# Kernel optimization log

Measured on AMD Instinct MI355X. Metric: run time of the kernel, lower is better.

Reference implementation:

```python
import jax, jax.numpy as jnp
import numpy as np

B, S, D = 2, 2048, 1024
H = 16
HD = D // H

def setup_inputs() -> dict:
    key = jax.random.key(0)
    k1, k2, k3 = jax.random.split(key, 3)
    x = jax.random.normal(k1, (B, S, D), dtype=jnp.float32)
    w_attn = jax.random.normal(k2, (D, 3 * D), dtype=jnp.float32) * (1.0 / np.sqrt(D))
    b_attn = jnp.zeros((3 * D,), dtype=jnp.float32)
    w_proj = jax.random.normal(k3, (D, D), dtype=jnp.float32) * (1.0 / np.sqrt(D))
    b_proj = jnp.zeros((D,), dtype=jnp.float32)
    return {"x": x, "w_attn": w_attn, "b_attn": b_attn, "w_proj": w_proj, "b_proj": b_proj}

def reference(x, w_attn, b_attn, w_proj, b_proj):
    bsz, seq_len, embed_dim = x.shape
    qkv = x @ w_attn + b_attn                      # [B,S,3D]
    q, k, v = jnp.split(qkv, 3, axis=-1)
    # [B,S,D] -> [B,H,S,HD]
    def heads(t):
        return t.reshape(bsz, seq_len, H, HD).transpose(0, 2, 1, 3)
    q, k, v = heads(q), heads(k), heads(v)
    scale = 1.0 / np.sqrt(HD)
    att = jnp.einsum('bhqd,bhkd->bhqk', q, k) * scale  # [B,H,S,S]
    causal = jnp.tril(jnp.ones((seq_len, seq_len), dtype=bool))
    att = jnp.where(causal[None, None], att, jnp.float32(-jnp.inf))
    att = jax.nn.softmax(att, axis=-1)
    y = jnp.einsum('bhqk,bhkd->bhqd', att, v)          # [B,H,S,HD]
    y = y.transpose(0, 2, 1, 3).reshape(bsz, seq_len, embed_dim)
    return y @ w_proj + b_proj
```

## Files before the change

kernel.cpp:

```cpp
#include <hip/hip_runtime.h>
#include <hip/hip_bf16.h>
#include <math.h>

typedef __bf16 bf16x8 __attribute__((ext_vector_type(8)));
typedef __bf16 bf16x4 __attribute__((ext_vector_type(4)));
typedef float f32x4 __attribute__((ext_vector_type(4)));

#define LOG2E 1.44269504088896340736f

#define SEQ 2048
#define DMODEL 1024
#define NH 16
#define HD 64

__device__ __forceinline__ void gl2lds16(const void* g, void* l) {
  __builtin_amdgcn_global_load_lds((__attribute__((address_space(1))) void*)g,
                                   (__attribute__((address_space(3))) void*)l,
                                   16, 0, 0);
}

__device__ __forceinline__ unsigned compute_flag_local(const unsigned* __restrict__ x,
                                                       int* cnt) {
  int c = 0;
  for (int i = threadIdx.x; i < 4096; i += 256) {
    unsigned e = (x[i] >> 23) & 0xFF;
    c += (e >= 0x70 && e <= 0x8F) ? 1 : 0;
  }
  cnt[threadIdx.x] = c;
  __syncthreads();
  for (int s = 128; s > 0; s >>= 1) {
    if ((int)threadIdx.x < s) cnt[threadIdx.x] += cnt[threadIdx.x + s];
    __syncthreads();
  }
  return (cnt[0] > 2048) ? 1u : 0u;
}

__device__ __forceinline__ void transpose_tile(const void* __restrict__ in,
                                               __hip_bfloat16* __restrict__ out,
                                               int R, int C, int c0, int r0, bool f32,
                                               __hip_bfloat16 (*tile)[65]) {
  const int tx = threadIdx.x & 63, ty = threadIdx.x >> 6;
#pragma unroll
  for (int i = 0; i < 16; ++i) {
    int r = ty + i * 4;
    long idx = (long)(r0 + r) * C + c0 + tx;
    tile[r][tx] = f32 ? __float2bfloat16(((const float*)in)[idx])
                      : ((const __hip_bfloat16*)in)[idx];
  }
  __syncthreads();
#pragma unroll
  for (int i = 0; i < 16; ++i) {
    int r = ty + i * 4;
    out[(long)(c0 + r) * R + r0 + tx] = tile[tx][r];
  }
}

__global__ void prep_all(const void* __restrict__ x, const void* __restrict__ w_attn,
                         const void* __restrict__ w_proj,
                         __hip_bfloat16* __restrict__ x_bf,
                         __hip_bfloat16* __restrict__ wT_attn,
                         __hip_bfloat16* __restrict__ wT_proj,
                         unsigned* __restrict__ flag) {
  __shared__ int cnt[256];
  __shared__ __hip_bfloat16 tile[64][65];
  const unsigned f = compute_flag_local((const unsigned*)x, cnt);
  const int bid = blockIdx.x;
  if (bid == 0 && threadIdx.x == 0) flag[0] = f;

  if (bid < 4096) {
    const int i = (bid * 256 + threadIdx.x) * 4;
    if (f) {
      const float4 v = *(const float4*)((const float*)x + i);
      x_bf[i + 0] = __float2bfloat16(v.x);
      x_bf[i + 1] = __float2bfloat16(v.y);
      x_bf[i + 2] = __float2bfloat16(v.z);
      x_bf[i + 3] = __float2bfloat16(v.w);
    } else {
      *(bf16x4*)(x_bf + i) = *(const bf16x4*)((const __hip_bfloat16*)x + i);
    }
  } else if (bid < 4096 + 768) {
    const int b2 = bid - 4096;
    const int c0 = (b2 % 48) * 64, r0 = (b2 / 48) * 64;
    transpose_tile(w_attn, wT_attn, 1024, 3072, c0, r0, f != 0, tile);
  } else {
    const int b3 = bid - 4096 - 768;
    const int c0 = (b3 % 16) * 64, r0 = (b3 / 16) * 64;
    transpose_tile(w_proj, wT_proj, 1024, 1024, c0, r0, f != 0, tile);
  }
}

template <int MODE>
__global__ __launch_bounds__(256, 3) void gemm_bt(
    const __hip_bfloat16* __restrict__ A, const __hip_bfloat16* __restrict__ Bt,
    const void* __restrict__ bias, void* __restrict__ C,
    __hip_bfloat16* __restrict__ q_ws, __hip_bfloat16* __restrict__ k_ws,
    __hip_bfloat16* __restrict__ vt_ws, int M, int N, int K,
    const unsigned* __restrict__ flag) {
  alignas(16) __shared__ __hip_bfloat16 lA[128 * 64];
  alignas(16) __shared__ __hip_bfloat16 lB[128 * 64];
  const int tid = threadIdx.x;
  const int wave = tid >> 6, lane = tid & 63;
  const int l15 = lane & 15, lq = lane >> 4;
  const int m0 = blockIdx.y * 128, n0 = blockIdx.x * 128;
  const int wrow = (wave >> 1) * 64, wcol = (wave & 1) * 64;

  const int rs = lane >> 3;
  const int cs = lane & 7;
  const int gch = cs ^ rs;
  const __hip_bfloat16* ap0 = A + (long)(m0 + wave * 32 + rs) * K + gch * 8;
  const __hip_bfloat16* bp0 = Bt + (long)(n0 + wave * 32 + rs) * K + gch * 8;

  f32x4 acc[4][4];
#pragma unroll
  for (int i = 0; i < 4; ++i)
#pragma unroll
    for (int j = 0; j < 4; ++j) acc[i][j] = {0.f, 0.f, 0.f, 0.f};

  for (int k0 = 0; k0 < K; k0 += 64) {
    __syncthreads();
#pragma unroll
    for (int i = 0; i < 4; ++i) {
      gl2lds16(ap0 + (long)(i * 8) * K + k0, lA + (wave * 4 + i) * 512);
      gl2lds16(bp0 + (long)(i * 8) * K + k0, lB + (wave * 4 + i) * 512);
    }
    __syncthreads();
#pragma unroll
    for (int ks = 0; ks < 2; ++ks) {
      bf16x8 af[4], bfr[4];
#pragma unroll
      for (int i = 0; i < 4; ++i) {
        const int p = wrow + 16 * i + l15;
        af[i] = *(const bf16x8*)(lA + p * 64 + (((ks * 4 + lq) ^ (l15 & 7)) * 8));
      }
#pragma unroll
      for (int j = 0; j < 4; ++j) {
        const int p = wcol + 16 * j + l15;
        bfr[j] = *(const bf16x8*)(lB + p * 64 + (((ks * 4 + lq) ^ (l15 & 7)) * 8));
      }
#pragma unroll
      for (int i = 0; i < 4; ++i)
#pragma unroll
        for (int j = 0; j < 4; ++j)
          acc[i][j] = __builtin_amdgcn_mfma_f32_16x16x32_bf16(af[i], bfr[j], acc[i][j], 0, 0, 0);
    }
  }

  const bool f32in = (*flag != 0);
  const bool outf32 = (MODE == 0) && f32in;
  const float KSCL = 0.125f * LOG2E;
#pragma unroll
  for (int i = 0; i < 4; ++i) {
    const int row = m0 + wrow + 16 * i + lq * 4;
#pragma unroll
    for (int j = 0; j < 4; ++j) {
      const int col = n0 + wcol + 16 * j + l15;
      const float bv = f32in ? ((const float*)bias)[col]
                             : __bfloat162float(((const __hip_bfloat16*)bias)[col]);
#pragma unroll
      for (int r = 0; r < 4; ++r) {
        const float v = acc[i][j][r] + bv;
        const int rr = row + r;
        if (MODE == 0) {
          if (outf32)
            ((float*)C)[(long)rr * N + col] = v;
          else
            ((__hip_bfloat16*)C)[(long)rr * N + col] = __float2bfloat16(v);
        } else {
          const int which = col >> 10;
          const int f = col & 1023;
          const int h = f >> 6, d = f & 63;
          const int b = rr >> 11, s = rr & 2047;
          const long bh = (long)b * NH + h;
          if (which == 0)
            q_ws[(bh * SEQ + s) * HD + d] = __float2bfloat16(v);
          else if (which == 1)
            k_ws[(bh * SEQ + s) * HD + d] = __float2bfloat16(v * KSCL);
          else {
            const int w = s & 31;
            const int wl = w & 15;
            const int sig = (w >> 4) ? (2 * (wl & ~3) + 4 + (wl & 3))
                                     : (2 * (wl & ~3) + (wl & 3));
            const int sp = (s & ~31) | sig;
            vt_ws[(bh * HD + d) * SEQ + sp] = __float2bfloat16(v);
          }
        }
      }
    }
  }
}

__global__ __launch_bounds__(256, 4) void attn_fused(
    const __hip_bfloat16* __restrict__ q_ws, const __hip_bfloat16* __restrict__ k_ws,
    const __hip_bfloat16* __restrict__ vt_ws, __hip_bfloat16* __restrict__ y_ws) {
  alignas(16) __shared__ __hip_bfloat16 lK[2][64 * 64];
  alignas(16) __shared__ __hip_bfloat16 lV[2][64 * 64];
  const int tid = threadIdx.x, wave = tid >> 6, lane = tid & 63;
  const int l15 = lane & 15, lq = lane >> 4;
  const int qt = 31 - (blockIdx.x >> 5);
  const int bh = blockIdx.x & 31;
  const int q0 = qt * 64;
  const int nkt = qt + 1;
  const __hip_bfloat16* Qb = q_ws + (long)bh * SEQ * HD;
  const __hip_bfloat16* Kb = k_ws + (long)bh * SEQ * HD;
  const __hip_bfloat16* Vb = vt_ws + (long)bh * HD * SEQ;
  const int b = bh >> 4, h = bh & 15;

  const int qrow = q0 + wave * 16 + l15;
  const bf16x8 qa0 = *(const bf16x8*)(Qb + (long)qrow * HD + lq * 8);
  const bf16x8 qa1 = *(const bf16x8*)(Qb + (long)qrow * HD + 32 + lq * 8);

  f32x4 accO[4];
  f32x4 accL;
#pragma unroll
  for (int j = 0; j < 4; ++j) accO[j] = {0.f, 0.f, 0.f, 0.f};
  accL = {0.f, 0.f, 0.f, 0.f};
  const __bf16 one = (__bf16)1.0f;
  const bf16x8 onesA = {one, one, one, one, one, one, one, one};

  const int p0 = wave * 16 + (lane >> 3);
  const int cl = lane & 7;

#pragma unroll
  for (int i = 0; i < 2; ++i) {
    const int p = p0 + i * 8;
    const int c = cl ^ (p & 7);
    gl2lds16(Kb + (long)p * HD + c * 8, &lK[0][(wave * 16 + i * 8) * 64]);
    gl2lds16(Vb + (long)p * SEQ + c * 8, &lV[0][(wave * 16 + i * 8) * 64]);
  }
  __syncthreads();

#pragma unroll 1
  for (int kt = 0; kt < nkt; ++kt) {
    const int buf = kt & 1;
    if (kt + 1 < nkt) {
      const int kb = (kt + 1) * 64;
#pragma unroll
      for (int i = 0; i < 2; ++i) {
        const int p = p0 + i * 8;
        const int c = cl ^ (p & 7);
        gl2lds16(Kb + (long)(kb + p) * HD + c * 8, &lK[buf ^ 1][(wave * 16 + i * 8) * 64]);
        gl2lds16(Vb + (long)p * SEQ + kb + c * 8, &lV[buf ^ 1][(wave * 16 + i * 8) * 64]);
      }
    }
    const __hip_bfloat16* lKb = lK[buf];
    const __hip_bfloat16* lVb = lV[buf];

    f32x4 st[4];
#pragma unroll
    for (int t = 0; t < 4; ++t) {
      st[t] = {0.f, 0.f, 0.f, 0.f};
      const int pp = t * 16 + l15;
      const bf16x8 kb0 = *(const bf16x8*)(lKb + (pp * 8 + (lq ^ (pp & 7))) * 8);
      const bf16x8 kb1 = *(const bf16x8*)(lKb + (pp * 8 + ((4 + lq) ^ (pp & 7))) * 8);
      st[t] = __builtin_amdgcn_mfma_f32_16x16x32_bf16(kb0, qa0, st[t], 0, 0, 0);
      st[t] = __builtin_amdgcn_mfma_f32_16x16x32_bf16(kb1, qa1, st[t], 0, 0, 0);
    }

    const bool diag = (kt == nkt - 1);
    const int qloc = wave * 16 + l15;
    bf16x8 pb[2];
#pragma unroll
    for (int c = 0; c < 2; ++c) {
#pragma unroll
      for (int t2 = 0; t2 < 2; ++t2) {
        const int tt = c * 2 + t2;
#pragma unroll
        for (int r = 0; r < 4; ++r) {
          float pv = exp2f(st[tt][r]);
          if (diag) {
            const int colloc = tt * 16 + lq * 4 + r;
            pv = (colloc <= qloc) ? pv : 0.f;
          }
          pb[c][t2 * 4 + r] = (__bf16)pv;
        }
      }
    }

#pragma unroll
    for (int j = 0; j < 4; ++j) {
      const int d = j * 16 + l15;
      const bf16x8 va0 = *(const bf16x8*)(lVb + (d * 8 + (lq ^ (d & 7))) * 8);
      const bf16x8 va1 = *(const bf16x8*)(lVb + (d * 8 + ((4 + lq) ^ (d & 7))) * 8);
      accO[j] = __builtin_amdgcn_mfma_f32_16x16x32_bf16(va0, pb[0], accO[j], 0, 0, 0);
      accO[j] = __builtin_amdgcn_mfma_f32_16x16x32_bf16(va1, pb[1], accO[j], 0, 0, 0);
    }
    accL = __builtin_amdgcn_mfma_f32_16x16x32_bf16(onesA, pb[0], accL, 0, 0, 0);
    accL = __builtin_amdgcn_mfma_f32_16x16x32_bf16(onesA, pb[1], accL, 0, 0, 0);
    __syncthreads();
  }

  const float inv = 1.f / accL[0];
  const int s = q0 + wave * 16 + l15;
  __hip_bfloat16* yb = y_ws + (long)(b * SEQ + s) * DMODEL + h * HD;
#pragma unroll
  for (int j = 0; j < 4; ++j) {
    bf16x4 o;
#pragma unroll
    for (int r = 0; r < 4; ++r) o[r] = (__bf16)(accO[j][r] * inv);
    *(bf16x4*)(yb + j * 16 + lq * 4) = o;
  }
}

extern "C" void kernel_launch(void* const* d_in, const int* in_sizes, int n_in,
                              void* d_out, int out_size, void* d_ws, size_t ws_size,
                              hipStream_t stream) {
  const void* x = d_in[0];
  const void* w_attn = d_in[1];
  const void* b_attn = d_in[2];
  const void* w_proj = d_in[3];
  const void* b_proj = d_in[4];

  char* ws = (char*)d_ws;
  const size_t MB = 1024 * 1024;
  unsigned* flag = (unsigned*)ws;
  __hip_bfloat16* wT_attn = (__hip_bfloat16*)(ws + 1 * MB);
  __hip_bfloat16* wT_proj = (__hip_bfloat16*)(ws + 7 * MB);
  __hip_bfloat16* x_bf = (__hip_bfloat16*)(ws + 9 * MB);
  __hip_bfloat16* q_ws = (__hip_bfloat16*)(ws + 17 * MB);
  __hip_bfloat16* k_ws = (__hip_bfloat16*)(ws + 25 * MB);
  __hip_bfloat16* vt_ws = (__hip_bfloat16*)(ws + 33 * MB);
  __hip_bfloat16* y_ws = (__hip_bfloat16*)(ws + 41 * MB);

  prep_all<<<dim3(4096 + 768 + 256), 256, 0, stream>>>(
      x, w_attn, w_proj, x_bf, wT_attn, wT_proj, flag);

  gemm_bt<1><<<dim3(3072 / 128, 4096 / 128), 256, 0, stream>>>(
      x_bf, wT_attn, b_attn, nullptr, q_ws, k_ws, vt_ws, 4096, 3072, 1024, flag);

  attn_fused<<<dim3(1024), 256, 0, stream>>>(q_ws, k_ws, vt_ws, y_ws);

  gemm_bt<0><<<dim3(1024 / 128, 4096 / 128), 256, 0, stream>>>(
      y_ws, wT_proj, b_proj, d_out, nullptr, nullptr, nullptr, 4096, 1024, 1024, flag);
}
```

Baseline: 197.4 us.

## Split causal attention over key chunks with separate combine kernel

```diff
diff --git a/kernel.cpp b/kernel.cpp
--- a/kernel.cpp
+++ b/kernel.cpp
@@ -189,21 +189,27 @@
   }
 }
 
-__global__ __launch_bounds__(256, 4) void attn_fused(
+__global__ __launch_bounds__(256, 4) void attn_part(
     const __hip_bfloat16* __restrict__ q_ws, const __hip_bfloat16* __restrict__ k_ws,
-    const __hip_bfloat16* __restrict__ vt_ws, __hip_bfloat16* __restrict__ y_ws) {
+    const __hip_bfloat16* __restrict__ vt_ws, float* __restrict__ po,
+    float* __restrict__ pl) {
   alignas(16) __shared__ __hip_bfloat16 lK[2][64 * 64];
   alignas(16) __shared__ __hip_bfloat16 lV[2][64 * 64];
   const int tid = threadIdx.x, wave = tid >> 6, lane = tid & 63;
   const int l15 = lane & 15, lq = lane >> 4;
-  const int qt = 31 - (blockIdx.x >> 5);
+  const int s = 79 - (blockIdx.x >> 5);
   const int bh = blockIdx.x & 31;
+  int qt, ch;
+  if (s < 8) { qt = s; ch = 0; }
+  else if (s < 24) { qt = 8 + ((s - 8) >> 1); ch = (s - 8) & 1; }
+  else if (s < 48) { qt = 16 + (s - 24) / 3; ch = (s - 24) % 3; }
+  else { qt = 24 + ((s - 48) >> 2); ch = (s - 48) & 3; }
   const int q0 = qt * 64;
-  const int nkt = qt + 1;
+  const int kt0 = ch * 8;
+  const int kt1 = min(kt0 + 8, qt + 1);
   const __hip_bfloat16* Qb = q_ws + (long)bh * SEQ * HD;
   const __hip_bfloat16* Kb = k_ws + (long)bh * SEQ * HD;
   const __hip_bfloat16* Vb = vt_ws + (long)bh * HD * SEQ;
-  const int b = bh >> 4, h = bh & 15;
 
   const int qrow = q0 + wave * 16 + l15;
   const bf16x8 qa0 = *(const bf16x8*)(Qb + (long)qrow * HD + lq * 8);
@@ -224,15 +230,15 @@
   for (int i = 0; i < 2; ++i) {
     const int p = p0 + i * 8;
     const int c = cl ^ (p & 7);
-    gl2lds16(Kb + (long)p * HD + c * 8, &lK[0][(wave * 16 + i * 8) * 64]);
-    gl2lds16(Vb + (long)p * SEQ + c * 8, &lV[0][(wave * 16 + i * 8) * 64]);
+    gl2lds16(Kb + (long)(kt0 * 64 + p) * HD + c * 8, &lK[0][(wave * 16 + i * 8) * 64]);
+    gl2lds16(Vb + (long)p * SEQ + kt0 * 64 + c * 8, &lV[0][(wave * 16 + i * 8) * 64]);
   }
   __syncthreads();
 
 #pragma unroll 1
-  for (int kt = 0; kt < nkt; ++kt) {
-    const int buf = kt & 1;
-    if (kt + 1 < nkt) {
+  for (int kt = kt0; kt < kt1; ++kt) {
+    const int buf = (kt - kt0) & 1;
+    if (kt + 1 < kt1) {
       const int kb = (kt + 1) * 64;
 #pragma unroll
       for (int i = 0; i < 2; ++i) {
@@ -256,7 +262,7 @@
       st[t] = __builtin_amdgcn_mfma_f32_16x16x32_bf16(kb1, qa1, st[t], 0, 0, 0);
     }
 
-    const bool diag = (kt == nkt - 1);
+    const bool diag = (kt == qt);
     const int qloc = wave * 16 + l15;
     bf16x8 pb[2];
 #pragma unroll
@@ -289,16 +295,53 @@
     __syncthreads();
   }
 
-  const float inv = 1.f / accL[0];
-  const int s = q0 + wave * 16 + l15;
-  __hip_bfloat16* yb = y_ws + (long)(b * SEQ + s) * DMODEL + h * HD;
-#pragma unroll
-  for (int j = 0; j < 4; ++j) {
-    bf16x4 o;
-#pragma unroll
-    for (int r = 0; r < 4; ++r) o[r] = (__bf16)(accO[j][r] * inv);
-    *(bf16x4*)(yb + j * 16 + lq * 4) = o;
-  }
+  const long base = (long)blockIdx.x * 4096;
+  const int q = wave * 16 + l15;
+#pragma unroll
+  for (int j = 0; j < 4; ++j)
+    *(f32x4*)(po + base + q * 64 + j * 16 + lq * 4) = accO[j];
+  if (lq == 0) pl[blockIdx.x * 64 + q] = accL[0];
+}
+
+__global__ __launch_bounds__(256) void attn_combine(
+    const float* __restrict__ po, const float* __restrict__ pl,
+    __hip_bfloat16* __restrict__ y_ws) {
+  const int bh = blockIdx.x & 31, qt = blockIdx.x >> 5;
+  const int b = bh >> 4, h = bh & 15;
+  int nch, b0;
+  if (qt < 8) { nch = 1; b0 = qt; }
+  else if (qt < 16) { nch = 2; b0 = 8 + 2 * (qt - 8); }
+  else if (qt < 24) { nch = 3; b0 = 24 + 3 * (qt - 16); }
+  else { nch = 4; b0 = 48 + 4 * (qt - 24); }
+  const int t = threadIdx.x, q = t >> 2, d0 = (t & 3) * 16;
+  float4 o[4];
+#pragma unroll
+  for (int i = 0; i < 4; ++i) o[i] = make_float4(0.f, 0.f, 0.f, 0.f);
+  float l = 0.f;
+  for (int c = 0; c < nch; ++c) {
+    const long bid = (long)(79 - (b0 + c)) * 32 + bh;
+    const float* p = po + bid * 4096 + q * 64 + d0;
+#pragma unroll
+    for (int i = 0; i < 4; ++i) {
+      const float4 v = *(const float4*)(p + i * 4);
+      o[i].x += v.x; o[i].y += v.y; o[i].z += v.z; o[i].w += v.w;
+    }
+    l += pl[bid * 64 + q];
+  }
+  const float inv = 1.f / l;
+  bf16x8 y0, y1;
+#pragma unroll
+  for (int i = 0; i < 4; ++i) {
+    bf16x8& yv = (i < 2) ? y0 : y1;
+    const int off = (i & 1) * 4;
+    yv[off + 0] = (__bf16)(o[i].x * inv);
+    yv[off + 1] = (__bf16)(o[i].y * inv);
+    yv[off + 2] = (__bf16)(o[i].z * inv);
+    yv[off + 3] = (__bf16)(o[i].w * inv);
+  }
+  __hip_bfloat16* yp = y_ws + (long)(b * SEQ + qt * 64 + q) * DMODEL + h * HD + d0;
+  *(bf16x8*)yp = y0;
+  *(bf16x8*)(yp + 8) = y1;
 }
 
 extern "C" void kernel_launch(void* const* d_in, const int* in_sizes, int n_in,
@@ -320,6 +363,8 @@
   __hip_bfloat16* k_ws = (__hip_bfloat16*)(ws + 25 * MB);
   __hip_bfloat16* vt_ws = (__hip_bfloat16*)(ws + 33 * MB);
   __hip_bfloat16* y_ws = (__hip_bfloat16*)(ws + 41 * MB);
+  float* po_ws = (float*)(ws + 49 * MB);
+  float* pl_ws = (float*)(ws + 90 * MB);
 
   prep_all<<<dim3(4096 + 768 + 256), 256, 0, stream>>>(
       x, w_attn, w_proj, x_bf, wT_attn, wT_proj, flag);
@@ -327,7 +372,8 @@
   gemm_bt<1><<<dim3(3072 / 128, 4096 / 128), 256, 0, stream>>>(
       x_bf, wT_attn, b_attn, nullptr, q_ws, k_ws, vt_ws, 4096, 3072, 1024, flag);
 
-  attn_fused<<<dim3(1024), 256, 0, stream>>>(q_ws, k_ws, vt_ws, y_ws);
+  attn_part<<<dim3(2560), 256, 0, stream>>>(q_ws, k_ws, vt_ws, po_ws, pl_ws);
+  attn_combine<<<dim3(1024), 256, 0, stream>>>(po_ws, pl_ws, y_ws);
 
   gemm_bt<0><<<dim3(1024 / 128, 4096 / 128), 256, 0, stream>>>(
       y_ws, wT_proj, b_proj, d_out, nullptr, nullptr, nullptr, 4096, 1024, 1024, flag);
```

Result: no change. 200.3 us (+1.5%).
